# Kernel optimization log

Hardware: AMD Instinct MI355X
Metric: run time of the kernel (lower is better)

Reference implementation:

```python
import jax, jax.numpy as jnp
import numpy as np

N_HEADS = 16
HIDDEN = 1024
HEAD = HIDDEN // N_HEADS


def setup_inputs() -> dict:
    key = jax.random.key(0)
    ks = jax.random.split(key, 11)
    B, S, H = 2, 2048, HIDDEN
    s = 1.0 / np.sqrt(H)
    return {
        "query": jax.random.normal(ks[0], (B, S, H), jnp.float32),
        "key": jax.random.normal(ks[1], (B, S, H), jnp.float32),
        "value": jax.random.normal(ks[2], (B, S, H), jnp.float32),
        "Wq": jax.random.normal(ks[3], (H, H), jnp.float32) * s,
        "bq": jnp.zeros((H,), jnp.float32),
        "Wk": jax.random.normal(ks[4], (H, H), jnp.float32) * s,
        "bk": jnp.zeros((H,), jnp.float32),
        "Wv": jax.random.normal(ks[5], (H, H), jnp.float32) * s,
        "bv": jnp.zeros((H,), jnp.float32),
        "Wo": jax.random.normal(ks[6], (H, H), jnp.float32) * s,
        "bo": jnp.zeros((H,), jnp.float32),
    }


def reference(query, key, value, Wq, bq, Wk, bk, Wv, bv, Wo, bo):
    B, Sq, H = query.shape
    Sk = key.shape[1]
    # QKV projections, split heads: [B, n_heads, S, head]
    q = (query @ Wq + bq).reshape(B, Sq, N_HEADS, HEAD).transpose(0, 2, 1, 3)
    k = (key @ Wk + bk).reshape(B, Sk, N_HEADS, HEAD).transpose(0, 2, 1, 3)
    v = (value @ Wv + bv).reshape(B, Sk, N_HEADS, HEAD).transpose(0, 2, 1, 3)
    # scaled dot-product attention (no mask, dropout p=0)
    scores = jnp.einsum("bhqd,bhkd->bhqk", q, k) / np.sqrt(HEAD).astype(np.float32)
    attn = jax.nn.softmax(scores, axis=-1)
    out = jnp.einsum("bhqk,bhkd->bhqd", attn, v)
    out = out.transpose(0, 2, 1, 3).reshape(B, Sq, H)
    return out @ Wo + bo
```

## Files before the change

### kernel.cpp

```cpp
#include <hip/hip_runtime.h>
#include <hip/hip_bf16.h>
#include <stdint.h>

typedef unsigned short u16;
typedef short bf16x8 __attribute__((ext_vector_type(8)));
typedef float f32x4 __attribute__((ext_vector_type(4)));

#define DEVI static __device__ __forceinline__

#if __has_builtin(__builtin_amdgcn_exp2f)
#define EXP2F(x) __builtin_amdgcn_exp2f(x)
#else
#define EXP2F(x) exp2f(x)
#endif

DEVI u16 f2bf(float f) {
  union { float f; uint32_t u; } v; v.f = f;
  uint32_t u = v.u;
  u += 0x7fffu + ((u >> 16) & 1u);
  return (u16)(u >> 16);
}
DEVI uint32_t fbits(float f) { union { float f; uint32_t u; } v; v.f = f; return v.u; }
DEVI float asf(uint32_t u)   { union { uint32_t u; float f; } v; v.u = u; return v.f; }

DEVI void async16(const void* g, const void* l) {
  __builtin_amdgcn_global_load_lds(
      (const __attribute__((address_space(1))) void*)g,
      (__attribute__((address_space(3))) void*)l, 16, 0, 0);
}

DEVI f32x4 mfma16(bf16x8 a, bf16x8 b, f32x4 c) {
  return __builtin_amdgcn_mfma_f32_16x16x32_bf16(a, b, c, 0, 0, 0);
}

#define CSC 0.18033688011112042f

__global__ void convx(const float* __restrict__ q, const float* __restrict__ k,
                      const float* __restrict__ v, u16* __restrict__ out) {
  const int z = blockIdx.y;
  const float* src = (z == 0) ? q : (z == 1) ? k : v;
  const int i = (blockIdx.x * 256 + threadIdx.x) * 4;
  float4 f = *(const float4*)(src + i);
  ushort4 o;
  o.x = f2bf(f.x); o.y = f2bf(f.y); o.z = f2bf(f.z); o.w = f2bf(f.w);
  *(ushort4*)(out + (size_t)z * 4194304 + i) = o;
}

__global__ void transw(const float* __restrict__ Wq, const float* __restrict__ Wk,
                       const float* __restrict__ Wv, const float* __restrict__ Wo,
                       u16* __restrict__ WT) {
  __shared__ u16 tile[64 * 68];
  const int z = blockIdx.z;
  const float* W = (z == 0) ? Wq : (z == 1) ? Wk : (z == 2) ? Wv : Wo;
  u16* out = WT + (size_t)z * 1048576;
  const int R0 = blockIdx.y * 64, C0 = blockIdx.x * 64;
  const int t = threadIdx.x;
#pragma unroll
  for (int it = 0; it < 16; ++it) {
    int j = it * 256 + t;
    int r = j >> 6, c = j & 63;
    tile[r * 68 + c] = f2bf(W[(size_t)(R0 + r) * 1024 + C0 + c]);
  }
  __syncthreads();
#pragma unroll
  for (int it = 0; it < 16; ++it) {
    int j = it * 256 + t;
    int c = j >> 6, r = j & 63;
    out[(size_t)(C0 + c) * 1024 + R0 + r] = tile[r * 68 + c];
  }
}

__global__ __launch_bounds__(256, 3)
void qkv_gemm(const u16* __restrict__ XB, const u16* __restrict__ WT,
              const float* __restrict__ bq, const float* __restrict__ bk,
              const float* __restrict__ bv,
              u16* __restrict__ QH, u16* __restrict__ KH, u16* __restrict__ VT) {
  __shared__ u16 lA[128 * 32];
  __shared__ u16 lB[128 * 32];
  const int z = blockIdx.z;
  const u16* A  = XB + (size_t)z * 4194304;
  const u16* Bt = WT + (size_t)z * 1048576;
  const float* bias = (z == 0) ? bq : (z == 1) ? bk : bv;
  const int t = threadIdx.x, lane = t & 63, w = t >> 6;
  const int quad = lane >> 4, l16 = lane & 15;
  const int wm = (w & 1) * 64, wn = (w >> 1) * 64;
  const int n0 = blockIdx.x * 128, m0 = blockIdx.y * 128;

  f32x4 acc[4][4] = {};
  for (int kt = 0; kt < 32; ++kt) {
    const int k0 = kt * 32;
#pragma unroll
    for (int it = 0; it < 2; ++it) {
      int i = it * 256 + w * 64 + lane;
      int r = i >> 2, cc = i & 3, c = cc ^ (r & 3);
      async16(A + (size_t)(m0 + r) * 1024 + k0 + c * 8, &lA[(it * 256 + w * 64) * 8]);
      async16(Bt + (size_t)(n0 + r) * 1024 + k0 + c * 8, &lB[(it * 256 + w * 64) * 8]);
    }
    __syncthreads();
    bf16x8 af[4], bfr[4];
#pragma unroll
    for (int rt = 0; rt < 4; ++rt) {
      int row = wm + rt * 16 + l16;
      af[rt] = *(const bf16x8*)&lA[row * 32 + (quad ^ (row & 3)) * 8];
    }
#pragma unroll
    for (int ct = 0; ct < 4; ++ct) {
      int row = wn + ct * 16 + l16;
      bfr[ct] = *(const bf16x8*)&lB[row * 32 + (quad ^ (row & 3)) * 8];
    }
#pragma unroll
    for (int rt = 0; rt < 4; ++rt)
#pragma unroll
      for (int ct = 0; ct < 4; ++ct)
        acc[rt][ct] = mfma16(af[rt], bfr[ct], acc[rt][ct]);
    __syncthreads();
  }

  float bvv[4];
  int ncol[4];
#pragma unroll
  for (int ct = 0; ct < 4; ++ct) {
    ncol[ct] = n0 + wn + ct * 16 + l16;
    bvv[ct] = bias[ncol[ct]];
  }
  if (z < 2) {
    u16* out = (z == 0) ? QH : KH;
    const float scl = (z == 0) ? CSC : 1.0f;
#pragma unroll
    for (int rt = 0; rt < 4; ++rt)
#pragma unroll
      for (int r = 0; r < 4; ++r) {
        int m = m0 + wm + rt * 16 + quad * 4 + r;
        int bb = m >> 11, s = m & 2047;
#pragma unroll
        for (int ct = 0; ct < 4; ++ct) {
          int hh = ncol[ct] >> 6, d = ncol[ct] & 63;
          out[((size_t)((bb * 16 + hh) * 2048 + s)) * 64 + d] =
              f2bf((acc[rt][ct][r] + bvv[ct]) * scl);
        }
      }
  } else {
#pragma unroll
    for (int rt = 0; rt < 4; ++rt) {
      int mb = m0 + wm + rt * 16 + quad * 4;
      int bb = mb >> 11, sb = mb & 2047;
#pragma unroll
      for (int ct = 0; ct < 4; ++ct) {
        int hh = ncol[ct] >> 6, d = ncol[ct] & 63;
        ushort4 pk;
        pk.x = f2bf(acc[rt][ct][0] + bvv[ct]);
        pk.y = f2bf(acc[rt][ct][1] + bvv[ct]);
        pk.z = f2bf(acc[rt][ct][2] + bvv[ct]);
        pk.w = f2bf(acc[rt][ct][3] + bvv[ct]);
        *(ushort4*)&VT[((size_t)((bb * 16 + hh) * 64 + d)) * 2048 + sb] = pk;
      }
    }
  }
}

__global__ __launch_bounds__(256, 2)
void attn2(const u16* __restrict__ QH, const u16* __restrict__ KH,
           const u16* __restrict__ VT, u16* __restrict__ AO) {
  __shared__ u16 lK[2][64 * 64];
  __shared__ u16 lV[2][64 * 64];
  __shared__ u16 lPT[4][32 * 64];
  const int qt0 = blockIdx.x, h = blockIdx.y, b = blockIdx.z;
  const int t = threadIdx.x, lane = t & 63, w = t >> 6;
  const int quad = lane >> 4, l16 = lane & 15;
  const u16* Qg = QH + ((size_t)((b * 16 + h) * 2048 + qt0 * 128)) * 64;
  const u16* Kg = KH + ((size_t)((b * 16 + h) * 2048)) * 64;
  const u16* Vg = VT + ((size_t)((b * 16 + h) * 64)) * 2048;

  bf16x8 qf[2][2];
#pragma unroll
  for (int qt = 0; qt < 2; ++qt)
#pragma unroll
    for (int ks = 0; ks < 2; ++ks)
      qf[qt][ks] = *(const bf16x8*)(Qg + (size_t)(w * 32 + qt * 16 + l16) * 64 +
                                    ks * 32 + quad * 8);

#pragma unroll
  for (int it = 0; it < 2; ++it) {
    int s = it * 256 + t;
    int r = s >> 3, cc = s & 7, c = cc ^ (r & 7);
    async16(Kg + (size_t)r * 64 + c * 8, &lK[0][s * 8]);
  }
#pragma unroll
  for (int it = 0; it < 2; ++it) {
    int s = it * 256 + t;
    int r = s >> 3, cc = s & 7, c = cc ^ (r & 7);
    async16(Vg + (size_t)r * 2048 + c * 8, &lV[0][s * 8]);
  }
  __syncthreads();

  f32x4 o[2][4] = {};
  float lsum[2] = {0.f, 0.f};
  const int swz = (l16 & 3) << 2;

  for (int kt = 0; kt < 32; ++kt) {
    const int cur = kt & 1, nxt = cur ^ 1;
    if (kt + 1 < 32) {
      const int kb = (kt + 1) * 64;
#pragma unroll
      for (int it = 0; it < 2; ++it) {
        int s = it * 256 + t;
        int r = s >> 3, cc = s & 7, c = cc ^ (r & 7);
        async16(Kg + (size_t)(kb + r) * 64 + c * 8, &lK[nxt][s * 8]);
      }
#pragma unroll
      for (int it = 0; it < 2; ++it) {
        int s = it * 256 + t;
        int r = s >> 3, cc = s & 7, c = cc ^ (r & 7);
        async16(Vg + (size_t)r * 2048 + kb + c * 8, &lV[nxt][s * 8]);
      }
    }

    f32x4 sc[2][4];
#pragma unroll
    for (int st = 0; st < 4; ++st) {
      int row = st * 16 + l16;
      bf16x8 kf0 = *(const bf16x8*)&lK[cur][row * 64 + ((quad) ^ (row & 7)) * 8];
      bf16x8 kf1 = *(const bf16x8*)&lK[cur][row * 64 + ((4 + quad) ^ (row & 7)) * 8];
      f32x4 z = {};
      sc[0][st] = mfma16(kf0, qf[0][0], z);
      sc[0][st] = mfma16(kf1, qf[0][1], sc[0][st]);
      sc[1][st] = mfma16(kf0, qf[1][0], z);
      sc[1][st] = mfma16(kf1, qf[1][1], sc[1][st]);
    }

#pragma unroll
    for (int qt = 0; qt < 2; ++qt) {
      int row = qt * 16 + l16;
      float part = 0.f;
#pragma unroll
      for (int st = 0; st < 4; ++st) {
        uint32_t a0 = fbits(EXP2F(sc[qt][st][0])) & 0xffff0000u;
        uint32_t a1 = fbits(EXP2F(sc[qt][st][1])) & 0xffff0000u;
        uint32_t a2 = fbits(EXP2F(sc[qt][st][2])) & 0xffff0000u;
        uint32_t a3 = fbits(EXP2F(sc[qt][st][3])) & 0xffff0000u;
        part += (asf(a0) + asf(a1)) + (asf(a2) + asf(a3));
        uint2 pk;
        pk.x = a1 | (a0 >> 16);
        pk.y = a3 | (a2 >> 16);
        int g = (st * 4 + quad) ^ swz;
        *(uint2*)&lPT[w][row * 64 + g * 4] = pk;
      }
      lsum[qt] += part;
    }

#pragma unroll
    for (int ks2 = 0; ks2 < 2; ++ks2) {
      int g0 = (ks2 * 8 + quad * 2) ^ swz;
      bf16x8 pf0 = *(const bf16x8*)&lPT[w][(l16) * 64 + g0 * 4];
      bf16x8 pf1 = *(const bf16x8*)&lPT[w][(16 + l16) * 64 + g0 * 4];
#pragma unroll
      for (int dt = 0; dt < 4; ++dt) {
        int row = dt * 16 + l16;
        bf16x8 vf = *(const bf16x8*)&lV[cur][row * 64 + ((ks2 * 4 + quad) ^ (row & 7)) * 8];
        o[0][dt] = mfma16(vf, pf0, o[0][dt]);
        o[1][dt] = mfma16(vf, pf1, o[1][dt]);
      }
    }
    __syncthreads();
  }

#pragma unroll
  for (int qt = 0; qt < 2; ++qt) {
    float l = lsum[qt];
    l += __shfl_xor(l, 16, 64);
    l += __shfl_xor(l, 32, 64);
    float inv = 1.0f / l;
    int qglob = qt0 * 128 + w * 32 + qt * 16 + l16;
    size_t base = ((size_t)(b * 2048 + qglob)) * 1024 + h * 64;
#pragma unroll
    for (int dt = 0; dt < 4; ++dt) {
      ushort4 pk;
      pk.x = f2bf(o[qt][dt][0] * inv);
      pk.y = f2bf(o[qt][dt][1] * inv);
      pk.z = f2bf(o[qt][dt][2] * inv);
      pk.w = f2bf(o[qt][dt][3] * inv);
      *(ushort4*)&AO[base + dt * 16 + quad * 4] = pk;
    }
  }
}

__global__ __launch_bounds__(256, 2)
void oproj_gemm(const u16* __restrict__ AO, const u16* __restrict__ Bt,
                const float* __restrict__ bias, float* __restrict__ out) {
  __shared__ u16 lA[128 * 32];
  __shared__ u16 lB[64 * 32];
  const int t = threadIdx.x, lane = t & 63, w = t >> 6;
  const int quad = lane >> 4, l16 = lane & 15;
  const int wm = (w & 1) * 64, wn = (w >> 1) * 32;
  const int n0 = blockIdx.x * 64, m0 = blockIdx.y * 128;

  f32x4 acc[4][2] = {};
  for (int kt = 0; kt < 32; ++kt) {
    const int k0 = kt * 32;
#pragma unroll
    for (int it = 0; it < 2; ++it) {
      int i = it * 256 + t;
      int r = i >> 2, cc = i & 3, c = cc ^ (r & 3);
      async16(AO + (size_t)(m0 + r) * 1024 + k0 + c * 8, &lA[i * 8]);
    }
    {
      int i = t;
      int r = i >> 2, cc = i & 3, c = cc ^ (r & 3);
      async16(Bt + (size_t)(n0 + r) * 1024 + k0 + c * 8, &lB[i * 8]);
    }
    __syncthreads();
    bf16x8 af[4], bfr[2];
#pragma unroll
    for (int rt = 0; rt < 4; ++rt) {
      int row = wm + rt * 16 + l16;
      af[rt] = *(const bf16x8*)&lA[row * 32 + (quad ^ (row & 3)) * 8];
    }
#pragma unroll
    for (int ct = 0; ct < 2; ++ct) {
      int row = wn + ct * 16 + l16;
      bfr[ct] = *(const bf16x8*)&lB[row * 32 + (quad ^ (row & 3)) * 8];
    }
#pragma unroll
    for (int rt = 0; rt < 4; ++rt)
#pragma unroll
      for (int ct = 0; ct < 2; ++ct)
        acc[rt][ct] = mfma16(af[rt], bfr[ct], acc[rt][ct]);
    __syncthreads();
  }

#pragma unroll
  for (int ct = 0; ct < 2; ++ct) {
    int ncol = n0 + wn + ct * 16 + l16;
    float bvv = bias[ncol];
#pragma unroll
    for (int rt = 0; rt < 4; ++rt)
#pragma unroll
      for (int r = 0; r < 4; ++r) {
        int m = m0 + wm + rt * 16 + quad * 4 + r;
        out[(size_t)m * 1024 + ncol] = acc[rt][ct][r] + bvv;
      }
  }
}

extern "C" void kernel_launch(void* const* d_in, const int* in_sizes, int n_in,
                              void* d_out, int out_size, void* d_ws, size_t ws_size,
                              hipStream_t stream) {
  const float* query = (const float*)d_in[0];
  const float* key   = (const float*)d_in[1];
  const float* value = (const float*)d_in[2];
  const float* Wq = (const float*)d_in[3];
  const float* bq = (const float*)d_in[4];
  const float* Wk = (const float*)d_in[5];
  const float* bk = (const float*)d_in[6];
  const float* Wv = (const float*)d_in[7];
  const float* bv = (const float*)d_in[8];
  const float* Wo = (const float*)d_in[9];
  const float* bo = (const float*)d_in[10];
  float* out = (float*)d_out;

  u16* WT = (u16*)d_ws;
  u16* QH = WT + 4 * 1048576;
  u16* KH = QH + 4194304;
  u16* VT = KH + 4194304;
  u16* XB = VT + 4194304;
  u16* AO = XB;

  convx<<<dim3(4096, 3), 256, 0, stream>>>(query, key, value, XB);
  transw<<<dim3(16, 16, 4), 256, 0, stream>>>(Wq, Wk, Wv, Wo, WT);
  qkv_gemm<<<dim3(8, 32, 3), 256, 0, stream>>>(XB, WT, bq, bk, bv, QH, KH, VT);
  attn2<<<dim3(16, 16, 2), 256, 0, stream>>>(QH, KH, VT, AO);
  oproj_gemm<<<dim3(16, 32), 256, 0, stream>>>(AO, WT + 3 * 1048576, bo, out);
}
```

Baseline: 240.1 us.

## Double GEMM K-tile depth and restructure attention to eight waves of sixteen queries

The QKV and output-projection GEMMs now stage 64-wide K tiles with an 8-way XOR swizzle, halving the number of barrier-separated iterations. The attention kernel moves to 512 threads, with each wave handling 16 query rows instead of 32. It uses a padded per-wave P buffer and converts P to bf16 with round-to-nearest packed conversions instead of truncation. These changes aim to cut synchronization overhead and raise wave-level parallelism, at the cost of more LDS per block and fewer independent MFMA chains per wave.

```diff
diff --git a/kernel.cpp b/kernel.cpp
--- a/kernel.cpp
+++ b/kernel.cpp
@@ -20,8 +20,10 @@
   u += 0x7fffu + ((u >> 16) & 1u);
   return (u16)(u >> 16);
 }
-DEVI uint32_t fbits(float f) { union { float f; uint32_t u; } v; v.f = f; return v.u; }
-DEVI float asf(uint32_t u)   { union { uint32_t u; float f; } v; v.u = u; return v.f; }
+DEVI uint32_t pk2bf(float lo, float hi) {
+  __hip_bfloat162 h = __float22bfloat162_rn(float2{lo, hi});
+  union { __hip_bfloat162 h; uint32_t u; } v; v.h = h; return v.u;
+}
 
 DEVI void async16(const void* g, const void* l) {
   __builtin_amdgcn_global_load_lds(
@@ -75,8 +77,8 @@
               const float* __restrict__ bq, const float* __restrict__ bk,
               const float* __restrict__ bv,
               u16* __restrict__ QH, u16* __restrict__ KH, u16* __restrict__ VT) {
-  __shared__ u16 lA[128 * 32];
-  __shared__ u16 lB[128 * 32];
+  __shared__ u16 lA[128 * 64];
+  __shared__ u16 lB[128 * 64];
   const int z = blockIdx.z;
   const u16* A  = XB + (size_t)z * 4194304;
   const u16* Bt = WT + (size_t)z * 1048576;
@@ -87,32 +89,35 @@
   const int n0 = blockIdx.x * 128, m0 = blockIdx.y * 128;
 
   f32x4 acc[4][4] = {};
-  for (int kt = 0; kt < 32; ++kt) {
-    const int k0 = kt * 32;
-#pragma unroll
-    for (int it = 0; it < 2; ++it) {
-      int i = it * 256 + w * 64 + lane;
-      int r = i >> 2, cc = i & 3, c = cc ^ (r & 3);
-      async16(A + (size_t)(m0 + r) * 1024 + k0 + c * 8, &lA[(it * 256 + w * 64) * 8]);
-      async16(Bt + (size_t)(n0 + r) * 1024 + k0 + c * 8, &lB[(it * 256 + w * 64) * 8]);
-    }
-    __syncthreads();
-    bf16x8 af[4], bfr[4];
-#pragma unroll
-    for (int rt = 0; rt < 4; ++rt) {
-      int row = wm + rt * 16 + l16;
-      af[rt] = *(const bf16x8*)&lA[row * 32 + (quad ^ (row & 3)) * 8];
-    }
-#pragma unroll
-    for (int ct = 0; ct < 4; ++ct) {
-      int row = wn + ct * 16 + l16;
-      bfr[ct] = *(const bf16x8*)&lB[row * 32 + (quad ^ (row & 3)) * 8];
-    }
-#pragma unroll
-    for (int rt = 0; rt < 4; ++rt)
-#pragma unroll
-      for (int ct = 0; ct < 4; ++ct)
-        acc[rt][ct] = mfma16(af[rt], bfr[ct], acc[rt][ct]);
+  for (int kt = 0; kt < 16; ++kt) {
+    const int k0 = kt * 64;
+#pragma unroll
+    for (int it = 0; it < 4; ++it) {
+      int i = it * 256 + t;
+      int r = i >> 3, cc = i & 7, c = cc ^ (r & 7);
+      async16(A + (size_t)(m0 + r) * 1024 + k0 + c * 8, &lA[i * 8]);
+      async16(Bt + (size_t)(n0 + r) * 1024 + k0 + c * 8, &lB[i * 8]);
+    }
+    __syncthreads();
+#pragma unroll
+    for (int ks = 0; ks < 2; ++ks) {
+      bf16x8 af[4], bfr[4];
+#pragma unroll
+      for (int rt = 0; rt < 4; ++rt) {
+        int row = wm + rt * 16 + l16;
+        af[rt] = *(const bf16x8*)&lA[row * 64 + ((ks * 4 + quad) ^ (row & 7)) * 8];
+      }
+#pragma unroll
+      for (int ct = 0; ct < 4; ++ct) {
+        int row = wn + ct * 16 + l16;
+        bfr[ct] = *(const bf16x8*)&lB[row * 64 + ((ks * 4 + quad) ^ (row & 7)) * 8];
+      }
+#pragma unroll
+      for (int rt = 0; rt < 4; ++rt)
+#pragma unroll
+        for (int ct = 0; ct < 4; ++ct)
+          acc[rt][ct] = mfma16(af[rt], bfr[ct], acc[rt][ct]);
+    }
     __syncthreads();
   }
 
@@ -158,12 +163,12 @@
   }
 }
 
-__global__ __launch_bounds__(256, 2)
-void attn2(const u16* __restrict__ QH, const u16* __restrict__ KH,
+__global__ __launch_bounds__(512, 4)
+void attn3(const u16* __restrict__ QH, const u16* __restrict__ KH,
            const u16* __restrict__ VT, u16* __restrict__ AO) {
   __shared__ u16 lK[2][64 * 64];
   __shared__ u16 lV[2][64 * 64];
-  __shared__ u16 lPT[4][32 * 64];
+  __shared__ u16 lPT[8][16 * 72];
   const int qt0 = blockIdx.x, h = blockIdx.y, b = blockIdx.z;
   const int t = threadIdx.x, lane = t & 63, w = t >> 6;
   const int quad = lane >> 4, l16 = lane & 15;
@@ -171,160 +176,130 @@
   const u16* Kg = KH + ((size_t)((b * 16 + h) * 2048)) * 64;
   const u16* Vg = VT + ((size_t)((b * 16 + h) * 64)) * 2048;
 
-  bf16x8 qf[2][2];
-#pragma unroll
-  for (int qt = 0; qt < 2; ++qt)
-#pragma unroll
-    for (int ks = 0; ks < 2; ++ks)
-      qf[qt][ks] = *(const bf16x8*)(Qg + (size_t)(w * 32 + qt * 16 + l16) * 64 +
-                                    ks * 32 + quad * 8);
-
-#pragma unroll
-  for (int it = 0; it < 2; ++it) {
-    int s = it * 256 + t;
-    int r = s >> 3, cc = s & 7, c = cc ^ (r & 7);
-    async16(Kg + (size_t)r * 64 + c * 8, &lK[0][s * 8]);
-  }
-#pragma unroll
-  for (int it = 0; it < 2; ++it) {
-    int s = it * 256 + t;
-    int r = s >> 3, cc = s & 7, c = cc ^ (r & 7);
-    async16(Vg + (size_t)r * 2048 + c * 8, &lV[0][s * 8]);
+  bf16x8 qf[2];
+#pragma unroll
+  for (int ks = 0; ks < 2; ++ks)
+    qf[ks] = *(const bf16x8*)(Qg + (size_t)(w * 16 + l16) * 64 + ks * 32 + quad * 8);
+
+  {
+    int r = t >> 3, cc = t & 7, c = cc ^ (r & 7);
+    async16(Kg + (size_t)r * 64 + c * 8, &lK[0][t * 8]);
+    async16(Vg + (size_t)r * 2048 + c * 8, &lV[0][t * 8]);
   }
   __syncthreads();
 
-  f32x4 o[2][4] = {};
-  float lsum[2] = {0.f, 0.f};
-  const int swz = (l16 & 3) << 2;
+  f32x4 o[4] = {};
+  float lsum = 0.f;
+  u16* myP = &lPT[w][0];
 
   for (int kt = 0; kt < 32; ++kt) {
     const int cur = kt & 1, nxt = cur ^ 1;
     if (kt + 1 < 32) {
       const int kb = (kt + 1) * 64;
-#pragma unroll
-      for (int it = 0; it < 2; ++it) {
-        int s = it * 256 + t;
-        int r = s >> 3, cc = s & 7, c = cc ^ (r & 7);
-        async16(Kg + (size_t)(kb + r) * 64 + c * 8, &lK[nxt][s * 8]);
-      }
-#pragma unroll
-      for (int it = 0; it < 2; ++it) {
-        int s = it * 256 + t;
-        int r = s >> 3, cc = s & 7, c = cc ^ (r & 7);
-        async16(Vg + (size_t)r * 2048 + kb + c * 8, &lV[nxt][s * 8]);
-      }
-    }
-
-    f32x4 sc[2][4];
+      int r = t >> 3, cc = t & 7, c = cc ^ (r & 7);
+      async16(Kg + (size_t)(kb + r) * 64 + c * 8, &lK[nxt][t * 8]);
+      async16(Vg + (size_t)r * 2048 + kb + c * 8, &lV[nxt][t * 8]);
+    }
+
+    f32x4 sc[4];
 #pragma unroll
     for (int st = 0; st < 4; ++st) {
       int row = st * 16 + l16;
       bf16x8 kf0 = *(const bf16x8*)&lK[cur][row * 64 + ((quad) ^ (row & 7)) * 8];
       bf16x8 kf1 = *(const bf16x8*)&lK[cur][row * 64 + ((4 + quad) ^ (row & 7)) * 8];
       f32x4 z = {};
-      sc[0][st] = mfma16(kf0, qf[0][0], z);
-      sc[0][st] = mfma16(kf1, qf[0][1], sc[0][st]);
-      sc[1][st] = mfma16(kf0, qf[1][0], z);
-      sc[1][st] = mfma16(kf1, qf[1][1], sc[1][st]);
-    }
-
-#pragma unroll
-    for (int qt = 0; qt < 2; ++qt) {
-      int row = qt * 16 + l16;
-      float part = 0.f;
-#pragma unroll
-      for (int st = 0; st < 4; ++st) {
-        uint32_t a0 = fbits(EXP2F(sc[qt][st][0])) & 0xffff0000u;
-        uint32_t a1 = fbits(EXP2F(sc[qt][st][1])) & 0xffff0000u;
-        uint32_t a2 = fbits(EXP2F(sc[qt][st][2])) & 0xffff0000u;
-        uint32_t a3 = fbits(EXP2F(sc[qt][st][3])) & 0xffff0000u;
-        part += (asf(a0) + asf(a1)) + (asf(a2) + asf(a3));
-        uint2 pk;
-        pk.x = a1 | (a0 >> 16);
-        pk.y = a3 | (a2 >> 16);
-        int g = (st * 4 + quad) ^ swz;
-        *(uint2*)&lPT[w][row * 64 + g * 4] = pk;
-      }
-      lsum[qt] += part;
+      sc[st] = mfma16(kf0, qf[0], z);
+      sc[st] = mfma16(kf1, qf[1], sc[st]);
+    }
+
+#pragma unroll
+    for (int st = 0; st < 4; ++st) {
+      float p0 = EXP2F(sc[st][0]);
+      float p1 = EXP2F(sc[st][1]);
+      float p2 = EXP2F(sc[st][2]);
+      float p3 = EXP2F(sc[st][3]);
+      lsum += (p0 + p1) + (p2 + p3);
+      uint2 pk;
+      pk.x = pk2bf(p0, p1);
+      pk.y = pk2bf(p2, p3);
+      *(uint2*)&myP[l16 * 72 + st * 16 + quad * 4] = pk;
     }
 
 #pragma unroll
     for (int ks2 = 0; ks2 < 2; ++ks2) {
-      int g0 = (ks2 * 8 + quad * 2) ^ swz;
-      bf16x8 pf0 = *(const bf16x8*)&lPT[w][(l16) * 64 + g0 * 4];
-      bf16x8 pf1 = *(const bf16x8*)&lPT[w][(16 + l16) * 64 + g0 * 4];
+      bf16x8 pf = *(const bf16x8*)&myP[l16 * 72 + ks2 * 32 + quad * 8];
 #pragma unroll
       for (int dt = 0; dt < 4; ++dt) {
         int row = dt * 16 + l16;
         bf16x8 vf = *(const bf16x8*)&lV[cur][row * 64 + ((ks2 * 4 + quad) ^ (row & 7)) * 8];
-        o[0][dt] = mfma16(vf, pf0, o[0][dt]);
-        o[1][dt] = mfma16(vf, pf1, o[1][dt]);
-      }
-    }
-    __syncthreads();
-  }
-
-#pragma unroll
-  for (int qt = 0; qt < 2; ++qt) {
-    float l = lsum[qt];
-    l += __shfl_xor(l, 16, 64);
-    l += __shfl_xor(l, 32, 64);
-    float inv = 1.0f / l;
-    int qglob = qt0 * 128 + w * 32 + qt * 16 + l16;
-    size_t base = ((size_t)(b * 2048 + qglob)) * 1024 + h * 64;
-#pragma unroll
-    for (int dt = 0; dt < 4; ++dt) {
-      ushort4 pk;
-      pk.x = f2bf(o[qt][dt][0] * inv);
-      pk.y = f2bf(o[qt][dt][1] * inv);
-      pk.z = f2bf(o[qt][dt][2] * inv);
-      pk.w = f2bf(o[qt][dt][3] * inv);
-      *(ushort4*)&AO[base + dt * 16 + quad * 4] = pk;
-    }
+        o[dt] = mfma16(vf, pf, o[dt]);
+      }
+    }
+    __syncthreads();
+  }
+
+  float l = lsum;
+  l += __shfl_xor(l, 16, 64);
+  l += __shfl_xor(l, 32, 64);
+  float inv = 1.0f / l;
+  int qglob = qt0 * 128 + w * 16 + l16;
+  size_t base = ((size_t)(b * 2048 + qglob)) * 1024 + h * 64;
+#pragma unroll
+  for (int dt = 0; dt < 4; ++dt) {
+    ushort4 pk;
+    pk.x = f2bf(o[dt][0] * inv);
+    pk.y = f2bf(o[dt][1] * inv);
+    pk.z = f2bf(o[dt][2] * inv);
+    pk.w = f2bf(o[dt][3] * inv);
+    *(ushort4*)&AO[base + dt * 16 + quad * 4] = pk;
   }
 }
 
 __global__ __launch_bounds__(256, 2)
 void oproj_gemm(const u16* __restrict__ AO, const u16* __restrict__ Bt,
                 const float* __restrict__ bias, float* __restrict__ out) {
-  __shared__ u16 lA[128 * 32];
-  __shared__ u16 lB[64 * 32];
+  __shared__ u16 lA[128 * 64];
+  __shared__ u16 lB[64 * 64];
   const int t = threadIdx.x, lane = t & 63, w = t >> 6;
   const int quad = lane >> 4, l16 = lane & 15;
   const int wm = (w & 1) * 64, wn = (w >> 1) * 32;
   const int n0 = blockIdx.x * 64, m0 = blockIdx.y * 128;
 
   f32x4 acc[4][2] = {};
-  for (int kt = 0; kt < 32; ++kt) {
-    const int k0 = kt * 32;
+  for (int kt = 0; kt < 16; ++kt) {
+    const int k0 = kt * 64;
+#pragma unroll
+    for (int it = 0; it < 4; ++it) {
+      int i = it * 256 + t;
+      int r = i >> 3, cc = i & 7, c = cc ^ (r & 7);
+      async16(AO + (size_t)(m0 + r) * 1024 + k0 + c * 8, &lA[i * 8]);
+    }
 #pragma unroll
     for (int it = 0; it < 2; ++it) {
       int i = it * 256 + t;
-      int r = i >> 2, cc = i & 3, c = cc ^ (r & 3);
-      async16(AO + (size_t)(m0 + r) * 1024 + k0 + c * 8, &lA[i * 8]);
-    }
-    {
-      int i = t;
-      int r = i >> 2, cc = i & 3, c = cc ^ (r & 3);
+      int r = i >> 3, cc = i & 7, c = cc ^ (r & 7);
       async16(Bt + (size_t)(n0 + r) * 1024 + k0 + c * 8, &lB[i * 8]);
     }
     __syncthreads();
-    bf16x8 af[4], bfr[2];
-#pragma unroll
-    for (int rt = 0; rt < 4; ++rt) {
-      int row = wm + rt * 16 + l16;
-      af[rt] = *(const bf16x8*)&lA[row * 32 + (quad ^ (row & 3)) * 8];
-    }
-#pragma unroll
-    for (int ct = 0; ct < 2; ++ct) {
-      int row = wn + ct * 16 + l16;
-      bfr[ct] = *(const bf16x8*)&lB[row * 32 + (quad ^ (row & 3)) * 8];
-    }
-#pragma unroll
-    for (int rt = 0; rt < 4; ++rt)
-#pragma unroll
-      for (int ct = 0; ct < 2; ++ct)
-        acc[rt][ct] = mfma16(af[rt], bfr[ct], acc[rt][ct]);
+#pragma unroll
+    for (int ks = 0; ks < 2; ++ks) {
+      bf16x8 af[4], bfr[2];
+#pragma unroll
+      for (int rt = 0; rt < 4; ++rt) {
+        int row = wm + rt * 16 + l16;
+        af[rt] = *(const bf16x8*)&lA[row * 64 + ((ks * 4 + quad) ^ (row & 7)) * 8];
+      }
+#pragma unroll
+      for (int ct = 0; ct < 2; ++ct) {
+        int row = wn + ct * 16 + l16;
+        bfr[ct] = *(const bf16x8*)&lB[row * 64 + ((ks * 4 + quad) ^ (row & 7)) * 8];
+      }
+#pragma unroll
+      for (int rt = 0; rt < 4; ++rt)
+#pragma unroll
+        for (int ct = 0; ct < 2; ++ct)
+          acc[rt][ct] = mfma16(af[rt], bfr[ct], acc[rt][ct]);
+    }
     __syncthreads();
   }
 
@@ -368,6 +343,6 @@
   convx<<<dim3(4096, 3), 256, 0, stream>>>(query, key, value, XB);
   transw<<<dim3(16, 16, 4), 256, 0, stream>>>(Wq, Wk, Wv, Wo, WT);
   qkv_gemm<<<dim3(8, 32, 3), 256, 0, stream>>>(XB, WT, bq, bk, bv, QH, KH, VT);
-  attn2<<<dim3(16, 16, 2), 256, 0, stream>>>(QH, KH, VT, AO);
+  attn3<<<dim3(16, 16, 2), 512, 0, stream>>>(QH, KH, VT, AO);
   oproj_gemm<<<dim3(16, 32), 256, 0, stream>>>(AO, WT + 3 * 1048576, bo, out);
 }
```

New measurement: 222.7 us. 7.2% less time.
